# Performance work log

Hardware: AMD Instinct MI355X
Metric: run time of the kernel (lower is better)

Reference implementation:

```python
import jax, jax.numpy as jnp
import numpy as np

N_BLOCKS = 8
N_WIRES = 24
GAMMA, BETA, ALPHA = 0.1, 0.6, 0.15


def _apply_ry(state, w, theta):
    # RY(theta) = [[cos(t/2), -sin(t/2)], [sin(t/2), cos(t/2)]] on wire w.
    c = jnp.cos(theta * 0.5)
    s = jnp.sin(theta * 0.5)
    st = jnp.moveaxis(state, w, 0)  # (2, ...)
    new = jnp.stack([c * st[0] - s * st[1], s * st[0] + c * st[1]])
    return jnp.moveaxis(new, 0, w)


def _apply_cnot(state, ctrl, tgt):
    # Flip target bit where control bit == 1.
    st = jnp.moveaxis(state, (ctrl, tgt), (0, 1))  # (2, 2, ...)
    new = jnp.stack([st[0], st[1, ::-1]])
    return jnp.moveaxis(new, (0, 1), (ctrl, tgt))


def setup_inputs() -> dict:
    key = jax.random.key(0)
    angles = jax.random.normal(key, (N_BLOCKS, N_WIRES), dtype=jnp.float32)
    return {"angles": angles}


def reference(angles):
    n_blocks, n_wires = angles.shape  # static
    # Initial state |0...0>; RY and CNOT are real, so the state stays real.
    state = jnp.zeros((2,) * n_wires, dtype=angles.dtype).at[(0,) * n_wires].set(1.0)
    for k in range(n_blocks):
        for w in range(n_wires):
            state = _apply_ry(state, w, angles[k, w])
        for w in range(n_wires - 1):  # circular=False -> linear chain
            state = _apply_cnot(state, w, w + 1)
    probs = (state.reshape(-1) ** 2).reshape(2 ** n_wires, 1)  # |amp|^2
    easy_scale = 2.0 ** (n_wires - 1)
    x = (BETA * jnp.tanh(GAMMA * easy_scale * probs)) ** ALPHA
    return x - jnp.mean(x)
```

## Files before the change

### kernel.cpp

```cpp
#include <hip/hip_runtime.h>

#define NW 24
#define NB 8
#define SSIZE (1u << 24)


__global__ void k_prep(const float* __restrict__ ang, float* __restrict__ ws) {
    int t = threadIdx.x;
    if (t == 0) ws[0] = 0.0f;
    if (t < NB * NW) {
        float a = 0.5f * ang[t];
        ws[64 + t]  = __builtin_cosf(a);
        ws[256 + t] = __builtin_sinf(a);
    }
}

__global__ void k_init(float* __restrict__ st, const float* __restrict__ ws) {
    const float* C = ws + 64;
    const float* S = ws + 256;
    unsigned q = blockIdx.x * blockDim.x + threadIdx.x;
    unsigned i = q << 2;
    unsigned jb = i ^ (i >> 1);
    float P = 1.0f;
#pragma unroll
    for (int b = 2; b < 24; ++b) {
        int w = 23 - b;
        P *= ((jb >> b) & 1) ? S[w] : C[w];
    }
    float4 v;
    float* vv = &v.x;
#pragma unroll
    for (int d = 0; d < 4; ++d) {
        unsigned ii = i + d;
        unsigned j = ii ^ (ii >> 1);
        float f1 = ((j >> 1) & 1) ? S[22] : C[22];
        float f0 = (j & 1)        ? S[23] : C[23];
        vv[d] = P * f1 * f0;
    }
    reinterpret_cast<float4*>(st)[q] = v;
}


__device__ __forceinline__ unsigned sw(unsigned f) { return f ^ ((f >> 3) & 7u); }

__device__ __forceinline__ void ry2(float& a0, float& a1, float c, float s, bool ctl) {
    float w0 = c * a0 - s * a1;
    float w1 = s * a0 + c * a1;
    a0 = ctl ? w1 : w0;
    a1 = ctl ? w0 : w1;
}

template<int TB, int MODE>
__device__ __forceinline__ void stage8(float4* x, float c, float s) {
#pragma unroll
    for (int j0 = 0; j0 < 8; ++j0) {
        if (j0 & (1 << TB)) continue;
        const int j1 = j0 | (1 << TB);
        const bool ctl = (MODE == 1) || (MODE == 0 && ((j0 >> (TB + 1)) & 1));
        ry2(x[j0].x, x[j1].x, c, s, ctl);
        ry2(x[j0].y, x[j1].y, c, s, ctl);
        ry2(x[j0].z, x[j1].z, c, s, ctl);
        ry2(x[j0].w, x[j1].w, c, s, ctl);
    }
}

__device__ __forceinline__ void low4(float4* y, const float* cc, const float* sv) {
    {
        float c = cc[2], s = sv[2];
        ry2(y[0].x, y[1].x, c, s, false); ry2(y[0].y, y[1].y, c, s, false);
        ry2(y[0].z, y[1].z, c, s, false); ry2(y[0].w, y[1].w, c, s, false);
        ry2(y[2].x, y[3].x, c, s, true);  ry2(y[2].y, y[3].y, c, s, true);
        ry2(y[2].z, y[3].z, c, s, true);  ry2(y[2].w, y[3].w, c, s, true);
    }
    {
        float c = cc[1], s = sv[1];
#pragma unroll
        for (int j = 0; j < 4; ++j) {
            bool ctl = j & 1;
            ry2(y[j].x, y[j].z, c, s, ctl);
            ry2(y[j].y, y[j].w, c, s, ctl);
        }
    }
    {
        float c = cc[0], s = sv[0];
#pragma unroll
        for (int j = 0; j < 4; ++j) {
            ry2(y[j].x, y[j].y, c, s, false);
            ry2(y[j].z, y[j].w, c, s, true);
        }
    }
}

template<int W>
__device__ __forceinline__ void gatherW(const float4* T4, unsigned tid, float4* x) {
    const unsigned lm = (1u << (W - 2)) - 1u;
    const unsigned fb = ((tid & ~lm) << 3) | (tid & lm);
#pragma unroll
    for (int j = 0; j < 8; ++j) x[j] = T4[sw(fb + (j << (W - 2)))];
}
template<int W>
__device__ __forceinline__ void scatterW(float4* T4, unsigned tid, const float4* x) {
    const unsigned lm = (1u << (W - 2)) - 1u;
    const unsigned fb = ((tid & ~lm) << 3) | (tid & lm);
#pragma unroll
    for (int j = 0; j < 8; ++j) T4[sw(fb + (j << (W - 2)))] = x[j];
}

__device__ __forceinline__ float xform(float v) {
    float z = 838860.8f * v * v;
    float e2 = __builtin_amdgcn_exp2f(z * 2.8853900817779268f);
    float big = 1.0f - 2.0f * __builtin_amdgcn_rcpf(e2 + 1.0f);
    float z2 = z * z;
    float small_ = z * (1.0f - 0.33333333f * z2 * (1.0f - 0.4f * z2));
    float t = (z < 0.04f) ? small_ : big;
    return __builtin_amdgcn_exp2f(0.15f * __builtin_amdgcn_logf(0.6f * t));
}

__global__ __launch_bounds__(512, 4) void k_passA(float* __restrict__ st,
                                                  float* __restrict__ ws,
                                                  int k, int fuse) {
    __shared__ float4 T4[4096];
    const unsigned m = blockIdx.x;
    const unsigned tid = threadIdx.x;
    const float* C = ws + 64 + k * 24;
    const float* S = ws + 256 + k * 24;
    float cc[14], sv[14];
#pragma unroll
    for (int b = 0; b < 14; ++b) { cc[b] = C[23 - b]; sv[b] = S[23 - b]; }

    float4* G4 = reinterpret_cast<float4*>(st) + (m << 12);
    float4 x[8];

#pragma unroll
    for (int j = 0; j < 8; ++j) x[j] = G4[tid + (j << 9)];
    if (m & 1u) stage8<2, 1>(x, cc[13], sv[13]);
    else        stage8<2,-1>(x, cc[13], sv[13]);
    stage8<1, 0>(x, cc[12], sv[12]);
    stage8<0, 0>(x, cc[11], sv[11]);
    scatterW<11>(T4, tid, x);
    __syncthreads();
    gatherW<9>(T4, tid, x);
    stage8<1, 0>(x, cc[10], sv[10]);
    stage8<0, 0>(x, cc[9],  sv[9]);
    scatterW<9>(T4, tid, x);
    __syncthreads();
    gatherW<7>(T4, tid, x);
    stage8<1, 0>(x, cc[8], sv[8]);
    stage8<0, 0>(x, cc[7], sv[7]);
    scatterW<7>(T4, tid, x);
    __syncthreads();
    gatherW<5>(T4, tid, x);
    stage8<1, 0>(x, cc[6], sv[6]);
    stage8<0, 0>(x, cc[5], sv[5]);
    scatterW<5>(T4, tid, x);
    __syncthreads();
    gatherW<3>(T4, tid, x);
    stage8<1, 0>(x, cc[4], sv[4]);
    stage8<0, 0>(x, cc[3], sv[3]);
    scatterW<3>(T4, tid, x);
    __syncthreads();
    const unsigned fb0 = tid << 2;
    const unsigned fb1 = (1u << 11) | (tid << 2);
#pragma unroll
    for (int j = 0; j < 4; ++j) x[j]     = T4[sw(fb0 + j)];
#pragma unroll
    for (int j = 0; j < 4; ++j) x[4 + j] = T4[sw(fb1 + j)];
    __syncthreads();
    low4(&x[0], cc, sv);
    low4(&x[4], cc, sv);
    if (fuse) {
        float lsum = 0.f;
#pragma unroll
        for (int j = 0; j < 8; ++j) {
            float* v = &x[j].x;
#pragma unroll
            for (int d = 0; d < 4; ++d) { v[d] = xform(v[d]); lsum += v[d]; }
        }
#pragma unroll
        for (int j = 0; j < 4; ++j) G4[fb0 + j] = x[j];
#pragma unroll
        for (int j = 0; j < 4; ++j) G4[fb1 + j] = x[4 + j];
#pragma unroll
        for (int o = 32; o > 0; o >>= 1) lsum += __shfl_down(lsum, o, 64);
        float* wsum = reinterpret_cast<float*>(T4);
        if ((tid & 63u) == 0) wsum[tid >> 6] = lsum;
        __syncthreads();
        if (tid == 0) {
            float b = 0.f;
#pragma unroll
            for (int i = 0; i < 8; ++i) b += wsum[i];
            atomicAdd(ws, b);
        }
    } else {
#pragma unroll
        for (int j = 0; j < 4; ++j) G4[fb0 + j] = x[j];
#pragma unroll
        for (int j = 0; j < 4; ++j) G4[fb1 + j] = x[4 + j];
    }
}

__global__ __launch_bounds__(512, 4) void k_passB(float* __restrict__ st,
                                                  const float* __restrict__ ws, int k) {
    __shared__ float4 T4[4096];
    const unsigned m = blockIdx.x;
    const unsigned tid = threadIdx.x;
    const float* C = ws + 64 + k * 24;
    const float* S = ws + 256 + k * 24;
    float cc[14], sv[14];
#pragma unroll
    for (int j = 4; j < 14; ++j) { cc[j] = C[13 - j]; sv[j] = S[13 - j]; }

    float4* G4 = reinterpret_cast<float4*>(st);
    const unsigned mb = m << 2;
    float4 x[8];

#pragma unroll
    for (int j = 0; j < 8; ++j) {
        unsigned f = tid | (j << 9);
        x[j] = G4[((f >> 2) << 12) | mb | (f & 3u)];
    }
    stage8<2,-1>(x, cc[13], sv[13]);
    stage8<1, 0>(x, cc[12], sv[12]);
    stage8<0, 0>(x, cc[11], sv[11]);
    scatterW<11>(T4, tid, x);
    __syncthreads();
    gatherW<9>(T4, tid, x);
    stage8<1, 0>(x, cc[10], sv[10]);
    stage8<0, 0>(x, cc[9],  sv[9]);
    scatterW<9>(T4, tid, x);
    __syncthreads();
    gatherW<7>(T4, tid, x);
    stage8<1, 0>(x, cc[8], sv[8]);
    stage8<0, 0>(x, cc[7], sv[7]);
    scatterW<7>(T4, tid, x);
    __syncthreads();
    gatherW<5>(T4, tid, x);
    stage8<1, 0>(x, cc[6], sv[6]);
    stage8<0, 0>(x, cc[5], sv[5]);
    scatterW<5>(T4, tid, x);
    __syncthreads();
    gatherW<3>(T4, tid, x);
    stage8<1, 0>(x, cc[4], sv[4]);
    scatterW<3>(T4, tid, x);
    __syncthreads();
#pragma unroll
    for (int i = 0; i < 8; ++i) {
        unsigned e = tid + (i << 9);
        G4[((e >> 2) << 12) | mb | (e & 3u)] = T4[sw(e)];
    }
}

__global__ void k_final(float* __restrict__ st, const float* __restrict__ ws) {
    unsigned idx = blockIdx.x * blockDim.x + threadIdx.x;
    unsigned stride = gridDim.x * blockDim.x;
    float mean = ws[0] * (1.0f / 16777216.0f);
    float4* G4 = reinterpret_cast<float4*>(st);
    for (unsigned q = idx; q < (SSIZE / 4); q += stride) {
        float4 v = G4[q];
        v.x -= mean; v.y -= mean; v.z -= mean; v.w -= mean;
        G4[q] = v;
    }
}

extern "C" void kernel_launch(void* const* d_in, const int* in_sizes, int n_in,
                              void* d_out, int out_size, void* d_ws, size_t ws_size,
                              hipStream_t stream) {
    const float* ang = (const float*)d_in[0];
    float* st = (float*)d_out;
    float* ws = (float*)d_ws;

    k_prep<<<1, 256, 0, stream>>>(ang, ws);
    k_init<<<16384, 256, 0, stream>>>(st, ws);
    for (int k = 1; k < NB; ++k) {
        k_passB<<<1024, 512, 0, stream>>>(st, ws, k);
        k_passA<<<1024, 512, 0, stream>>>(st, ws, k, (k == NB - 1) ? 1 : 0);
    }
    k_final<<<4096, 256, 0, stream>>>(st, ws);
}
```

Before: 617.0 us.

## Use 16 float4 per thread with 256 threads, fewer LDS rounds, fuse init into first pass

Each thread now holds 16 float4 values instead of 8, with 256-thread blocks. This lets each register stage apply 3-4 wire rotations between LDS exchanges, so there are fewer scatter/gather rounds and barriers per pass. The separate k_init kernel is removed and the product-state initialization is computed in registers inside the first passB, saving a full write and read of the state vector. The LDS swizzle changes to match the new access patterns. Register pressure rises, and launch bounds drop occupancy to 2 blocks.

```diff
diff --git a/kernel.cpp b/kernel.cpp
--- a/kernel.cpp
+++ b/kernel.cpp
@@ -1,6 +1,5 @@
 #include <hip/hip_runtime.h>
 
-#define NW 24
 #define NB 8
 #define SSIZE (1u << 24)
 
@@ -8,40 +7,17 @@
 __global__ void k_prep(const float* __restrict__ ang, float* __restrict__ ws) {
     int t = threadIdx.x;
     if (t == 0) ws[0] = 0.0f;
-    if (t < NB * NW) {
+    if (t < NB * 24) {
         float a = 0.5f * ang[t];
         ws[64 + t]  = __builtin_cosf(a);
         ws[256 + t] = __builtin_sinf(a);
     }
 }
 
-__global__ void k_init(float* __restrict__ st, const float* __restrict__ ws) {
-    const float* C = ws + 64;
-    const float* S = ws + 256;
-    unsigned q = blockIdx.x * blockDim.x + threadIdx.x;
-    unsigned i = q << 2;
-    unsigned jb = i ^ (i >> 1);
-    float P = 1.0f;
-#pragma unroll
-    for (int b = 2; b < 24; ++b) {
-        int w = 23 - b;
-        P *= ((jb >> b) & 1) ? S[w] : C[w];
-    }
-    float4 v;
-    float* vv = &v.x;
-#pragma unroll
-    for (int d = 0; d < 4; ++d) {
-        unsigned ii = i + d;
-        unsigned j = ii ^ (ii >> 1);
-        float f1 = ((j >> 1) & 1) ? S[22] : C[22];
-        float f0 = (j & 1)        ? S[23] : C[23];
-        vv[d] = P * f1 * f0;
-    }
-    reinterpret_cast<float4*>(st)[q] = v;
-}
-
-
-__device__ __forceinline__ unsigned sw(unsigned f) { return f ^ ((f >> 3) & 7u); }
+
+__device__ __forceinline__ unsigned sw(unsigned f) {
+    return f ^ (((f >> 3) ^ (f >> 5)) & 7u);
+}
 
 __device__ __forceinline__ void ry2(float& a0, float& a1, float c, float s, bool ctl) {
     float w0 = c * a0 - s * a1;
@@ -51,9 +27,9 @@
 }
 
 template<int TB, int MODE>
-__device__ __forceinline__ void stage8(float4* x, float c, float s) {
-#pragma unroll
-    for (int j0 = 0; j0 < 8; ++j0) {
+__device__ __forceinline__ void stage16(float4* x, float c, float s) {
+#pragma unroll
+    for (int j0 = 0; j0 < 16; ++j0) {
         if (j0 & (1 << TB)) continue;
         const int j1 = j0 | (1 << TB);
         const bool ctl = (MODE == 1) || (MODE == 0 && ((j0 >> (TB + 1)) & 1));
@@ -64,46 +40,16 @@
     }
 }
 
-__device__ __forceinline__ void low4(float4* y, const float* cc, const float* sv) {
-    {
-        float c = cc[2], s = sv[2];
-        ry2(y[0].x, y[1].x, c, s, false); ry2(y[0].y, y[1].y, c, s, false);
-        ry2(y[0].z, y[1].z, c, s, false); ry2(y[0].w, y[1].w, c, s, false);
-        ry2(y[2].x, y[3].x, c, s, true);  ry2(y[2].y, y[3].y, c, s, true);
-        ry2(y[2].z, y[3].z, c, s, true);  ry2(y[2].w, y[3].w, c, s, true);
-    }
-    {
-        float c = cc[1], s = sv[1];
-#pragma unroll
-        for (int j = 0; j < 4; ++j) {
-            bool ctl = j & 1;
-            ry2(y[j].x, y[j].z, c, s, ctl);
-            ry2(y[j].y, y[j].w, c, s, ctl);
-        }
-    }
-    {
-        float c = cc[0], s = sv[0];
-#pragma unroll
-        for (int j = 0; j < 4; ++j) {
-            ry2(y[j].x, y[j].y, c, s, false);
-            ry2(y[j].z, y[j].w, c, s, true);
-        }
-    }
-}
-
-template<int W>
-__device__ __forceinline__ void gatherW(const float4* T4, unsigned tid, float4* x) {
-    const unsigned lm = (1u << (W - 2)) - 1u;
-    const unsigned fb = ((tid & ~lm) << 3) | (tid & lm);
-#pragma unroll
-    for (int j = 0; j < 8; ++j) x[j] = T4[sw(fb + (j << (W - 2)))];
-}
-template<int W>
-__device__ __forceinline__ void scatterW(float4* T4, unsigned tid, const float4* x) {
-    const unsigned lm = (1u << (W - 2)) - 1u;
-    const unsigned fb = ((tid & ~lm) << 3) | (tid & lm);
-#pragma unroll
-    for (int j = 0; j < 8; ++j) T4[sw(fb + (j << (W - 2)))] = x[j];
+__device__ __forceinline__ void dstages(float4* x, float c1, float s1,
+                                        float c0, float s0) {
+#pragma unroll
+    for (int j = 0; j < 16; ++j) {
+        bool ctl = j & 1;
+        ry2(x[j].x, x[j].z, c1, s1, ctl);
+        ry2(x[j].y, x[j].w, c1, s1, ctl);
+        ry2(x[j].x, x[j].y, c0, s0, false);
+        ry2(x[j].z, x[j].w, c0, s0, true);
+    }
 }
 
 __device__ __forceinline__ float xform(float v) {
@@ -116,7 +62,7 @@
     return __builtin_amdgcn_exp2f(0.15f * __builtin_amdgcn_logf(0.6f * t));
 }
 
-__global__ __launch_bounds__(512, 4) void k_passA(float* __restrict__ st,
+__global__ __launch_bounds__(256, 2) void k_passA(float* __restrict__ st,
                                                   float* __restrict__ ws,
                                                   int k, int fuse) {
     __shared__ float4 T4[4096];
@@ -124,129 +70,172 @@
     const unsigned tid = threadIdx.x;
     const float* C = ws + 64 + k * 24;
     const float* S = ws + 256 + k * 24;
-    float cc[14], sv[14];
-#pragma unroll
-    for (int b = 0; b < 14; ++b) { cc[b] = C[23 - b]; sv[b] = S[23 - b]; }
+    float ca[14], sa[14];
+#pragma unroll
+    for (int b = 0; b < 14; ++b) { ca[b] = C[23 - b]; sa[b] = S[23 - b]; }
 
     float4* G4 = reinterpret_cast<float4*>(st) + (m << 12);
-    float4 x[8];
-
-#pragma unroll
-    for (int j = 0; j < 8; ++j) x[j] = G4[tid + (j << 9)];
-    if (m & 1u) stage8<2, 1>(x, cc[13], sv[13]);
-    else        stage8<2,-1>(x, cc[13], sv[13]);
-    stage8<1, 0>(x, cc[12], sv[12]);
-    stage8<0, 0>(x, cc[11], sv[11]);
-    scatterW<11>(T4, tid, x);
-    __syncthreads();
-    gatherW<9>(T4, tid, x);
-    stage8<1, 0>(x, cc[10], sv[10]);
-    stage8<0, 0>(x, cc[9],  sv[9]);
-    scatterW<9>(T4, tid, x);
-    __syncthreads();
-    gatherW<7>(T4, tid, x);
-    stage8<1, 0>(x, cc[8], sv[8]);
-    stage8<0, 0>(x, cc[7], sv[7]);
-    scatterW<7>(T4, tid, x);
-    __syncthreads();
-    gatherW<5>(T4, tid, x);
-    stage8<1, 0>(x, cc[6], sv[6]);
-    stage8<0, 0>(x, cc[5], sv[5]);
-    scatterW<5>(T4, tid, x);
-    __syncthreads();
-    gatherW<3>(T4, tid, x);
-    stage8<1, 0>(x, cc[4], sv[4]);
-    stage8<0, 0>(x, cc[3], sv[3]);
-    scatterW<3>(T4, tid, x);
-    __syncthreads();
-    const unsigned fb0 = tid << 2;
-    const unsigned fb1 = (1u << 11) | (tid << 2);
-#pragma unroll
-    for (int j = 0; j < 4; ++j) x[j]     = T4[sw(fb0 + j)];
-#pragma unroll
-    for (int j = 0; j < 4; ++j) x[4 + j] = T4[sw(fb1 + j)];
-    __syncthreads();
-    low4(&x[0], cc, sv);
-    low4(&x[4], cc, sv);
-    if (fuse) {
-        float lsum = 0.f;
-#pragma unroll
-        for (int j = 0; j < 8; ++j) {
-            float* v = &x[j].x;
-#pragma unroll
-            for (int d = 0; d < 4; ++d) { v[d] = xform(v[d]); lsum += v[d]; }
-        }
-#pragma unroll
-        for (int j = 0; j < 4; ++j) G4[fb0 + j] = x[j];
-#pragma unroll
-        for (int j = 0; j < 4; ++j) G4[fb1 + j] = x[4 + j];
-#pragma unroll
-        for (int o = 32; o > 0; o >>= 1) lsum += __shfl_down(lsum, o, 64);
-        float* wsum = reinterpret_cast<float*>(T4);
-        if ((tid & 63u) == 0) wsum[tid >> 6] = lsum;
-        __syncthreads();
-        if (tid == 0) {
-            float b = 0.f;
-#pragma unroll
-            for (int i = 0; i < 8; ++i) b += wsum[i];
-            atomicAdd(ws, b);
-        }
-    } else {
-#pragma unroll
-        for (int j = 0; j < 4; ++j) G4[fb0 + j] = x[j];
-#pragma unroll
-        for (int j = 0; j < 4; ++j) G4[fb1 + j] = x[4 + j];
-    }
-}
-
-__global__ __launch_bounds__(512, 4) void k_passB(float* __restrict__ st,
-                                                  const float* __restrict__ ws, int k) {
+    float4 x[16];
+
+#pragma unroll
+    for (int jj = 0; jj < 16; ++jj) x[jj] = G4[tid + (jj << 8)];
+    if (m & 1u) stage16<3, 1>(x, ca[13], sa[13]);
+    else        stage16<3,-1>(x, ca[13], sa[13]);
+    stage16<2, 0>(x, ca[12], sa[12]);
+    stage16<1, 0>(x, ca[11], sa[11]);
+    stage16<0, 0>(x, ca[10], sa[10]);
+#pragma unroll
+    for (int jj = 0; jj < 16; ++jj) T4[sw(tid | (jj << 8))] = x[jj];
+    __syncthreads();
+    {
+        const unsigned fb = (tid & 31) | ((tid >> 5) << 9);
+#pragma unroll
+        for (int jj = 0; jj < 16; ++jj) x[jj] = T4[sw(fb | (jj << 5))];
+        stage16<2, 0>(x, ca[9], sa[9]);
+        stage16<1, 0>(x, ca[8], sa[8]);
+        stage16<0, 0>(x, ca[7], sa[7]);
+#pragma unroll
+        for (int jj = 0; jj < 16; ++jj) T4[sw(fb | (jj << 5))] = x[jj];
+    }
+    __syncthreads();
+    {
+        const unsigned fb = (tid & 3) | ((tid >> 2) << 6);
+#pragma unroll
+        for (int jj = 0; jj < 16; ++jj) x[jj] = T4[sw(fb | (jj << 2))];
+        stage16<2, 0>(x, ca[6], sa[6]);
+        stage16<1, 0>(x, ca[5], sa[5]);
+        stage16<0, 0>(x, ca[4], sa[4]);
+#pragma unroll
+        for (int jj = 0; jj < 16; ++jj) T4[sw(fb | (jj << 2))] = x[jj];
+    }
+    __syncthreads();
+    {
+#pragma unroll
+        for (int jj = 0; jj < 16; ++jj)
+            x[jj] = T4[sw((jj & 7) | (tid << 3) | ((jj >> 3) << 11))];
+        stage16<1, 0>(x, ca[3], sa[3]);
+        stage16<0, 0>(x, ca[2], sa[2]);
+        dstages(x, ca[1], sa[1], ca[0], sa[0]);
+        if (fuse) {
+            float lsum = 0.f;
+#pragma unroll
+            for (int jj = 0; jj < 16; ++jj) {
+                float* v = &x[jj].x;
+#pragma unroll
+                for (int d = 0; d < 4; ++d) { v[d] = xform(v[d]); lsum += v[d]; }
+            }
+#pragma unroll
+            for (int jj = 0; jj < 16; ++jj)
+                G4[(jj & 7) | (tid << 3) | ((jj >> 3) << 11)] = x[jj];
+#pragma unroll
+            for (int o = 32; o > 0; o >>= 1) lsum += __shfl_down(lsum, o, 64);
+            __syncthreads();
+            float* wsum = reinterpret_cast<float*>(T4);
+            if ((tid & 63u) == 0) wsum[tid >> 6] = lsum;
+            __syncthreads();
+            if (tid == 0)
+                atomicAdd(ws, wsum[0] + wsum[1] + wsum[2] + wsum[3]);
+        } else {
+#pragma unroll
+            for (int jj = 0; jj < 16; ++jj)
+                G4[(jj & 7) | (tid << 3) | ((jj >> 3) << 11)] = x[jj];
+        }
+    }
+}
+
+__global__ __launch_bounds__(256, 2) void k_passB(float* __restrict__ st,
+                                                  const float* __restrict__ ws,
+                                                  int k, int init) {
     __shared__ float4 T4[4096];
     const unsigned m = blockIdx.x;
     const unsigned tid = threadIdx.x;
     const float* C = ws + 64 + k * 24;
     const float* S = ws + 256 + k * 24;
-    float cc[14], sv[14];
-#pragma unroll
-    for (int j = 4; j < 14; ++j) { cc[j] = C[13 - j]; sv[j] = S[13 - j]; }
+    float cg[10], sg[10];
+#pragma unroll
+    for (int t = 0; t < 10; ++t) { cg[t] = C[9 - t]; sg[t] = S[9 - t]; }
 
     float4* G4 = reinterpret_cast<float4*>(st);
     const unsigned mb = m << 2;
-    float4 x[8];
-
-#pragma unroll
-    for (int j = 0; j < 8; ++j) {
-        unsigned f = tid | (j << 9);
-        x[j] = G4[((f >> 2) << 12) | mb | (f & 3u)];
-    }
-    stage8<2,-1>(x, cc[13], sv[13]);
-    stage8<1, 0>(x, cc[12], sv[12]);
-    stage8<0, 0>(x, cc[11], sv[11]);
-    scatterW<11>(T4, tid, x);
-    __syncthreads();
-    gatherW<9>(T4, tid, x);
-    stage8<1, 0>(x, cc[10], sv[10]);
-    stage8<0, 0>(x, cc[9],  sv[9]);
-    scatterW<9>(T4, tid, x);
-    __syncthreads();
-    gatherW<7>(T4, tid, x);
-    stage8<1, 0>(x, cc[8], sv[8]);
-    stage8<0, 0>(x, cc[7], sv[7]);
-    scatterW<7>(T4, tid, x);
-    __syncthreads();
-    gatherW<5>(T4, tid, x);
-    stage8<1, 0>(x, cc[6], sv[6]);
-    stage8<0, 0>(x, cc[5], sv[5]);
-    scatterW<5>(T4, tid, x);
-    __syncthreads();
-    gatherW<3>(T4, tid, x);
-    stage8<1, 0>(x, cc[4], sv[4]);
-    scatterW<3>(T4, tid, x);
-    __syncthreads();
-#pragma unroll
-    for (int i = 0; i < 8; ++i) {
-        unsigned e = tid + (i << 9);
-        G4[((e >> 2) << 12) | mb | (e & 3u)] = T4[sw(e)];
+    float4 x[16];
+
+    if (init) {
+        const float* C0 = ws + 64;
+        const float* S0 = ws + 256;
+        unsigned t2 = tid & 3u;
+        unsigned th = tid >> 2;
+        float P = 1.f;
+        { unsigned g = (t2 ^ (t2 >> 1)) & 1u;      P *= g ? S0[21] : C0[21]; }
+        { unsigned g = ((t2 >> 1) ^ m) & 1u;       P *= g ? S0[20] : C0[20]; }
+#pragma unroll
+        for (int b = 4; b <= 12; ++b) {
+            unsigned g = ((m >> (b - 4)) ^ (m >> (b - 3))) & 1u;
+            P *= g ? S0[23 - b] : C0[23 - b];
+        }
+        { unsigned g = ((m >> 9) ^ th) & 1u;       P *= g ? S0[10] : C0[10]; }
+#pragma unroll
+        for (int b = 14; b <= 18; ++b) {
+            unsigned g = ((th >> (b - 14)) ^ (th >> (b - 13))) & 1u;
+            P *= g ? S0[23 - b] : C0[23 - b];
+        }
+        float D[4];
+#pragma unroll
+        for (int d = 0; d < 4; ++d) {
+            unsigned g0 = (d ^ (d >> 1)) & 1u;
+            unsigned g1 = ((d >> 1) ^ t2) & 1u;
+            D[d] = (g0 ? S0[23] : C0[23]) * (g1 ? S0[22] : C0[22]);
+        }
+        unsigned th5 = (th >> 5) & 1u;
+#pragma unroll
+        for (int jj = 0; jj < 16; ++jj) {
+            unsigned g19 = (th5 ^ (unsigned)jj) & 1u;
+            unsigned g20 = ((unsigned)jj ^ ((unsigned)jj >> 1)) & 1u;
+            unsigned g21 = (((unsigned)jj >> 1) ^ ((unsigned)jj >> 2)) & 1u;
+            unsigned g22 = (((unsigned)jj >> 2) ^ ((unsigned)jj >> 3)) & 1u;
+            unsigned g23 = ((unsigned)jj >> 3) & 1u;
+            float J = (g19 ? S0[4] : C0[4]) * (g20 ? S0[3] : C0[3]) *
+                      (g21 ? S0[2] : C0[2]) * (g22 ? S0[1] : C0[1]) *
+                      (g23 ? S0[0] : C0[0]);
+            float PJ = P * J;
+            x[jj] = make_float4(PJ * D[0], PJ * D[1], PJ * D[2], PJ * D[3]);
+        }
+    } else {
+#pragma unroll
+        for (int jj = 0; jj < 16; ++jj) {
+            unsigned lf = tid | (jj << 8);
+            x[jj] = G4[((lf >> 2) << 12) | mb | (lf & 3u)];
+        }
+    }
+    stage16<3,-1>(x, cg[9], sg[9]);
+    stage16<2, 0>(x, cg[8], sg[8]);
+    stage16<1, 0>(x, cg[7], sg[7]);
+    stage16<0, 0>(x, cg[6], sg[6]);
+#pragma unroll
+    for (int jj = 0; jj < 16; ++jj) T4[sw(tid | (jj << 8))] = x[jj];
+    __syncthreads();
+    {
+        const unsigned fb = (tid & 31) | ((tid >> 5) << 9);
+#pragma unroll
+        for (int jj = 0; jj < 16; ++jj) x[jj] = T4[sw(fb | (jj << 5))];
+        stage16<2, 0>(x, cg[5], sg[5]);
+        stage16<1, 0>(x, cg[4], sg[4]);
+        stage16<0, 0>(x, cg[3], sg[3]);
+#pragma unroll
+        for (int jj = 0; jj < 16; ++jj) T4[sw(fb | (jj << 5))] = x[jj];
+    }
+    __syncthreads();
+    {
+        const unsigned fb = (tid & 3) | ((tid >> 2) << 6);
+#pragma unroll
+        for (int jj = 0; jj < 16; ++jj) x[jj] = T4[sw(fb | (jj << 2))];
+        stage16<2, 0>(x, cg[2], sg[2]);
+        stage16<1, 0>(x, cg[1], sg[1]);
+        stage16<0, 0>(x, cg[0], sg[0]);
+#pragma unroll
+        for (int jj = 0; jj < 16; ++jj) {
+            unsigned lf = fb | (jj << 2);
+            G4[((lf >> 2) << 12) | mb | (lf & 3u)] = x[jj];
+        }
     }
 }
 
@@ -270,10 +259,9 @@
     float* ws = (float*)d_ws;
 
     k_prep<<<1, 256, 0, stream>>>(ang, ws);
-    k_init<<<16384, 256, 0, stream>>>(st, ws);
     for (int k = 1; k < NB; ++k) {
-        k_passB<<<1024, 512, 0, stream>>>(st, ws, k);
-        k_passA<<<1024, 512, 0, stream>>>(st, ws, k, (k == NB - 1) ? 1 : 0);
+        k_passB<<<1024, 256, 0, stream>>>(st, ws, k, (k == 1) ? 1 : 0);
+        k_passA<<<1024, 256, 0, stream>>>(st, ws, k, (k == NB - 1) ? 1 : 0);
     }
     k_final<<<4096, 256, 0, stream>>>(st, ws);
 }
```

New measurement: 613.1 us. Within noise of the previous version (-0.6%).
